# Optimization experiments

Hardware: AMD Instinct MI355X
Metric: run time of the kernel (lower is better)

Reference implementation:

```python
import jax, jax.numpy as jnp
import numpy as np

# dataset '25' constants
NBC = 30; DX = 10; NT = 1000; DT = 0.0008; FREQ = 25
SX = np.linspace(0, 99, num=10) * 10.0
SZ = 10.0
GX = np.linspace(0, 99, num=100) * 10.0
GZ = 10.0
SAMPLE_RATIO = 1
C1, C2, C3 = -2.5, 4.0 / 3.0, -1.0 / 12.0


def ricker(f, dt, nt):
    nw = 2.2 / f / dt
    nw = 2 * np.floor(nw / 2) + 1
    nc = np.floor(nw / 2)
    k = np.arange(nw)
    alpha = (nc - k) * f * dt * np.pi
    beta = alpha ** 2
    w0 = (1 - 2 * beta) * np.exp(-beta)
    w = np.zeros(nt)
    w[: len(w0)] = w0
    return jnp.asarray(w, dtype=jnp.float32)


def get_abc(vp, nbc, dx):
    B = vp.shape[0]
    velmin = jnp.min(vp.reshape(B, -1), axis=-1)              # [B]
    a = (nbc - 1) * dx
    kappa = 3.0 * velmin * np.float32(np.log(1e7)) / (2.0 * a)  # [B]
    prof = kappa[:, None] * (jnp.arange(nbc, dtype=vp.dtype) * dx / a) ** 2  # [B, nbc]
    pf = prof[:, ::-1]
    damp = jnp.zeros_like(vp)
    damp = damp.at[:, :, :nbc, :].set(pf[:, None, :, None])
    damp = damp.at[:, :, -nbc:, :].set(prof[:, None, :, None])
    damp = damp.at[:, :, :, :nbc].set(pf[:, None, None, :])
    damp = damp.at[:, :, :, -nbc:].set(prof[:, None, None, :])
    return damp


def fwm(v):
    # v: padded velocity [B, 1, nz_pad, nx_pad]
    src = ricker(FREQ, DT, NT)                                # [NT]
    alpha = (v * DT / DX) ** 2
    kappa = get_abc(v, NBC, DX) * DT
    temp1 = 2.0 + 2.0 * C1 * alpha - kappa
    temp2 = 1.0 - kappa
    beta_dt = (v * DT) ** 2

    isx = (np.around(SX / DX) + NBC).astype(int)              # [ns]
    isz = int(np.around(SZ / DX)) + NBC
    igx = (np.around(GX / DX) + NBC).astype(int)              # [ng]
    igz = int(np.around(GZ / DX)) + NBC
    ns = len(isx)

    B, nz, nx = v.shape[0], v.shape[2], v.shape[3]
    src_amp = beta_dt[:, 0, isz, isx]                         # [B, ns]
    loc = jnp.arange(ns)
    isx_j = jnp.asarray(isx)

    def step(carry, s):
        p0, p1 = carry                                        # each [B, ns, nz, nx]
        lap = C2 * (jnp.roll(p1, 1, -2) + jnp.roll(p1, -1, -2)
                    + jnp.roll(p1, 1, -1) + jnp.roll(p1, -1, -1)) \
            + C3 * (jnp.roll(p1, 2, -2) + jnp.roll(p1, -2, -2)
                    + jnp.roll(p1, 2, -1) + jnp.roll(p1, -2, -1))
        p = temp1 * p1 - temp2 * p0 + alpha * lap
        p = p.at[:, loc, isz, isx_j].add(src_amp * s)         # per-shot source injection
        rec = p[:, :, igz, igx]                               # [B, ns, ng]
        return (p1, p), rec

    p_init = jnp.zeros((B, ns, nz, nx), v.dtype)
    _, recs = jax.lax.scan(step, (p_init, p_init), src)       # recs: [NT, B, ns, ng]
    seis = jnp.transpose(recs, (1, 2, 0, 3))[:, :, ::SAMPLE_RATIO, :]
    return seis


def setup_inputs() -> dict:
    key = jax.random.key(0)
    v = jax.random.uniform(key, (1, 1, 70, 100), dtype=jnp.float32)
    return {"v": v}


def reference(v):
    v_denorm = v * 1000.0 + 3000.0                            # v_denorm_func
    v_pad = jnp.pad(v_denorm, ((0, 0), (0, 0), (NBC, NBC), (NBC, NBC)), mode="edge")
    seis = fwm(v_pad)                                         # [B, ns, NT, ng]
    return seis                                               # s_norm_func = identity
```

## Files before the change

kernel.cpp:

```cpp
#include <hip/hip_runtime.h>
#include <math.h>


#define SROW 168
#define PS_ROWS 52
#define PSZ (PS_ROWS * SROW)
#define RH 2
#define DTf 0.0008f
#define C2f 1.3333333333333333f
#define C3f (-0.08333333333333333f)

#define CST_OFF 4096
#define G_OFF   262144
#define FLAG_OFF 3590144
#define GSEG 10400

#define LD4(arr, i) (*reinterpret_cast<const float4*>(&(arr)[i]))
#define LD2(arr, i) (*reinterpret_cast<const float2*>(&(arr)[i]))
#define ST4(arr, i, v) (*reinterpret_cast<float4*>(&(arr)[i]) = (v))

__global__ __launch_bounds__(1024) void fwi_setup1(const float* __restrict__ v,
                                                   float* __restrict__ ws,
                                                   unsigned int* __restrict__ flags) {
    int tid = threadIdx.x;
    if (tid < 80) flags[tid] = 0u;
    float m = 3.402823466e38f;
    for (int i = tid; i < 7000; i += 1024) m = fminf(m, v[i]);
    #pragma unroll
    for (int off = 32; off > 0; off >>= 1) m = fminf(m, __shfl_down(m, off, 64));
    __shared__ float red[16];
    if ((tid & 63) == 0) red[tid >> 6] = m;
    __syncthreads();
    if (tid == 0) {
        float mm = red[0];
        for (int i = 1; i < 16; ++i) mm = fminf(mm, red[i]);
        ws[1010] = mm * 1000.0f + 3000.0f;
    }
    if (tid < 1000) {
        float w = 0.0f;
        if (tid < 111) {
            float a = (float)(55 - tid) * 0.06283185307179587f;
            float b = a * a;
            w = (1.0f - 2.0f * b) * expf(-b);
        }
        ws[tid] = w;
    }
    if (tid >= 1000 && tid < 1010) {
        int l = tid - 1000;
        float vd = v[100 + 11 * l] * 1000.0f + 3000.0f;
        float bdt = vd * DTf;
        ws[tid] = bdt * bdt;
    }
}

__global__ __launch_bounds__(256) void fwi_setup2(const float* __restrict__ v,
                                                  const float* __restrict__ ws,
                                                  float* __restrict__ CST) {
    int c = blockIdx.x * 256 + threadIdx.x;
    if (c >= 130 * 160) return;
    float velmin = ws[1010];
    int z = c / 160;
    int x = c - z * 160;
    int iz = min(max(z - 30, 0), 69);
    int ix = min(max(x - 30, 0), 99);
    float vd = v[iz * 100 + ix] * 1000.0f + 3000.0f;
    float tt = vd * DTf / 10.0f;
    float al = tt * tt;
    int qx = max(29 - x, x - 130);
    int qz = max(29 - z, z - 100);
    int q = (qx >= 0) ? qx : qz;
    float kdt = 0.0f;
    if (q >= 0) {
        float kap3 = 3.0f * velmin * 16.118095650958319f / 580.0f;
        float r = (float)q * (10.0f / 290.0f);
        kdt = kap3 * (r * r) * DTf;
    }
    int quad = c >> 2, j = c & 3;
    CST[quad * 12 + j]     = al;
    CST[quad * 12 + 4 + j] = 2.0f - 5.0f * al - kdt;
    CST[quad * 12 + 8 + j] = kdt - 1.0f;
}

static __device__ __forceinline__ float cellq(float l2, float l1, float cc, float r1, float r2,
                                              float u1, float u2, float d1, float d2,
                                              float al, float t1, float t2n, float p0) {
    float lap = C2f * ((l1 + r1) + (u1 + d1)) + C3f * ((l2 + r2) + (u2 + d2));
    return (t1 * cc + t2n * p0) + al * lap;
}

static __device__ __forceinline__ float4 ld_remote16(const unsigned long long* p) {
    union { unsigned long long u; float2 f; } a, b;
    a.u = __hip_atomic_load(p,     __ATOMIC_RELAXED, __HIP_MEMORY_SCOPE_AGENT);
    b.u = __hip_atomic_load(p + 1, __ATOMIC_RELAXED, __HIP_MEMORY_SCOPE_AGENT);
    return make_float4(a.f.x, a.f.y, b.f.x, b.f.y);
}
static __device__ __forceinline__ void st_remote16(unsigned long long* p, float4 v) {
    union { unsigned long long u; float2 f; } c;
    c.f = make_float2(v.x, v.y);
    __hip_atomic_store(p,     c.u, __ATOMIC_RELAXED, __HIP_MEMORY_SCOPE_AGENT);
    c.f = make_float2(v.z, v.w);
    __hip_atomic_store(p + 1, c.u, __ATOMIC_RELAXED, __HIP_MEMORY_SCOPE_AGENT);
}

#define ROWQ4(q, c, p0, hl, hr, u1, u2, d1, d2, al4, t14, t24) do {             \
    (q).x = cellq((hl).x, (hl).y, (c).x, (c).y, (c).z,                          \
                  (u1).x, (u2).x, (d1).x, (d2).x, (al4).x, (t14).x, (t24).x, (p0).x); \
    (q).y = cellq((hl).y, (c).x, (c).y, (c).z, (c).w,                           \
                  (u1).y, (u2).y, (d1).y, (d2).y, (al4).y, (t14).y, (t24).y, (p0).y); \
    (q).z = cellq((c).x, (c).y, (c).z, (c).w, (hr).x,                           \
                  (u1).z, (u2).z, (d1).z, (d2).z, (al4).z, (t14).z, (t24).z, (p0).z); \
    (q).w = cellq((c).y, (c).z, (c).w, (hr).x, (hr).y,                          \
                  (u1).w, (u2).w, (d1).w, (d2).w, (al4).w, (t14).w, (t24).w, (p0).w); \
} while (0)

#define STEP(CUR, OLD, T, K, PR, PW) do {                                       \
    const int Ti = (T);                                                         \
    const int kp1 = (K) + 1;                                                    \
    const bool actk = act && (gr >= (ct ? kp1 : 0)) && (gr < ng - (cb ? kp1 : 0)); \
    const float as = (Ti < 111) ? amp * Wv[Ti] : 0.0f;                          \
    if (actk) {                                                                 \
        float4 hu2 = LD4(PR, pc0 - 2 * SROW);                                   \
        float4 hu1 = LD4(PR, pc0 - SROW);                                       \
        float4 hd1 = LD4(PR, pc0 + 2 * SROW);                                   \
        float4 hd2 = LD4(PR, pc0 + 3 * SROW);                                   \
        float2 hl0 = LD2(PR, pc0 - 2);                                          \
        float2 hr0 = LD2(PR, pc0 + 4);                                          \
        float2 hl1 = LD2(PR, pc0 + SROW - 2);                                   \
        float2 hr1 = LD2(PR, pc0 + SROW + 4);                                   \
        float4 q0, q1;                                                          \
        ROWQ4(q0, (CUR)[0], (OLD)[0], hl0, hr0, hu1, hu2, (CUR)[1], hd1, ca0, ct0, cs0); \
        ROWQ4(q1, (CUR)[1], (OLD)[1], hl1, hr1, (CUR)[0], hu1, hd1, hd2, ca1, ct1, cs1); \
        if (src0) {                                 \
            q0.x += (ls == 0) ? as : 0.0f;                                      \
            q0.y += (ls == 1) ? as : 0.0f;                                      \
            q0.z += (ls == 2) ? as : 0.0f;                                      \
            q0.w += (ls == 3) ? as : 0.0f;                                      \
        }                                                                       \
        if (src1) {                                 \
            q1.x += (ls == 0) ? as : 0.0f;                                      \
            q1.y += (ls == 1) ? as : 0.0f;                                      \
            q1.z += (ls == 2) ? as : 0.0f;                                      \
            q1.w += (ls == 3) ? as : 0.0f;                                      \
        }                                                                       \
        if (grec) {                                 \
            const int ob = shot * 100000 + Ti * 100 + xr0;                      \
            if (xr0 >= 0  && xr0 <= 99) out[ob]     = q1.x;                     \
            if (xr0 >= -1 && xr0 <= 98) out[ob + 1] = q1.y;                     \
            if (xr0 >= -2 && xr0 <= 97) out[ob + 2] = q1.z;                     \
            if (xr0 >= -3 && xr0 <= 96) out[ob + 3] = q1.w;                     \
        }                                                                       \
        (OLD)[0] = q0; (OLD)[1] = q1;                                           \
        ST4(PW, pc0, q0);                                                       \
        ST4(PW, pc0 + SROW, q1);                                                \
    }                                                                           \
    __syncthreads();                            \
} while (0)

#define EXCHANGE(E) do {                                                        \
    const int par = (E) & 1;                                                    \
    if (act) {                                                                  \
        _Pragma("unroll")                                                       \
        for (int r = 0; r < RH; ++r) {                                          \
            int slot = gr * 2 + r;                                              \
            if (slot >= halo_top && slot < halo_top + int_n) {                  \
                int grow = base + slot;                                         \
                size_t b1 = ((size_t)(par*2+0)*10 + shot)*GSEG + (size_t)grow*80 + 2*qx; \
                size_t b0 = ((size_t)(par*2+1)*10 + shot)*GSEG + (size_t)grow*80 + 2*qx; \
                st_remote16(Gu + b1, pB[r]);                                    \
                st_remote16(Gu + b0, pA[r]);                                    \
            }                                                                   \
        }                                                                       \
    }                                                                           \
    __syncthreads();                                       \
    if (tid == 0)                                                               \
        __hip_atomic_store(&flags[(shot << 3) + seg], (unsigned)(E) + 1u,       \
                           __ATOMIC_RELEASE, __HIP_MEMORY_SCOPE_AGENT);         \
    if (tid == 64 && seg > 0)                                                   \
        while (__hip_atomic_load(&flags[(shot << 3) + seg - 1], __ATOMIC_ACQUIRE,\
                                 __HIP_MEMORY_SCOPE_AGENT) <= (unsigned)(E)) {} \
    if (tid == 128 && seg < 7)                                                  \
        while (__hip_atomic_load(&flags[(shot << 3) + seg + 1], __ATOMIC_ACQUIRE,\
                                 __HIP_MEMORY_SCOPE_AGENT) <= (unsigned)(E)) {} \
    __syncthreads();                                 \
    if (act) {                                                                  \
        _Pragma("unroll")                                                       \
        for (int r = 0; r < RH; ++r) {                                          \
            int slot = gr * 2 + r;                                              \
            if (slot < halo_top || slot >= halo_top + int_n) {                  \
                int grow = base + slot;                                         \
                size_t b1 = ((size_t)(par*2+0)*10 + shot)*GSEG + (size_t)grow*80 + 2*qx; \
                size_t b0 = ((size_t)(par*2+1)*10 + shot)*GSEG + (size_t)grow*80 + 2*qx; \
                float4 v1 = ld_remote16(Gu + b1);                               \
                float4 v0 = ld_remote16(Gu + b0);                               \
                pB[r] = v1;                                                     \
                pA[r] = v0;                                                     \
                ST4(PsA, pc0 + r * SROW, v1);                                   \
            }                                                                   \
        }                                                                       \
    }                                                                           \
    __syncthreads();                             \
} while (0)

__global__ __launch_bounds__(1024, 4) void fwi_main(const float4* __restrict__ CST4,
                                                    const float* __restrict__ ws,
                                                    unsigned long long* __restrict__ Gu,
                                                    unsigned int* __restrict__ flags,
                                                    float* __restrict__ out) {
    __shared__ float PsA[PSZ];
    __shared__ float PsB[PSZ];
    __shared__ float Wv[1024];
    const int tid = threadIdx.x;
    const int bid = blockIdx.x;
    const int shot = bid >> 3, seg = bid & 7;

    for (int i = tid; i < PSZ; i += 1024) { PsA[i] = 0.0f; PsB[i] = 0.0f; }
    Wv[tid] = (tid < 111) ? ws[tid] : 0.0f;

    const int int_base = 16 * seg;
    const int int_n = (seg < 7) ? 16 : 18;
    const int base = (seg > 0) ? int_base - 16 : 0;
    const int halo_top = (seg > 0) ? 16 : 0;
    const int stored_n = halo_top + int_n + ((seg < 7) ? 16 : 0);
    const bool ct = (seg > 0);
    const bool cb = (seg < 7);
    const int ng = stored_n >> 1;

    const int gr = tid / 40;
    const int qx = tid - gr * 40;
    const bool act = (gr < 24) && (gr * 2 < stored_n);
    const float amp = ws[1000 + shot];
    const int xs = 30 + 11 * shot;
    const bool isq = (qx == (xs >> 2));
    const int ls = xs & 3;
    const int s31 = 31 - base;
    const bool src0 = act && isq && (gr * 2 == s31);
    const bool src1 = act && isq && (gr * 2 + 1 == s31);
    const int pc0 = (gr * 2 + 2) * SROW + 4 * qx + 4;
    const float4* cst = CST4 + (size_t)((base + gr * 2) * 40 + qx) * 3;
    const bool grec = (seg == 1) && (gr == 15);
    const int xr0 = 4 * qx - 30;

    float4 ca0, ct0, cs0, ca1, ct1, cs1;
    ca0 = ct0 = cs0 = ca1 = ct1 = cs1 = make_float4(0.f, 0.f, 0.f, 0.f);
    if (act) {
        ca0 = cst[0];   ct0 = cst[1];   cs0 = cst[2];
        ca1 = cst[120]; ct1 = cst[121]; cs1 = cst[122];
    }

    float4 pA[RH], pB[RH];
    #pragma unroll
    for (int r = 0; r < RH; ++r) {
        pA[r] = make_float4(0.f, 0.f, 0.f, 0.f);
        pB[r] = make_float4(0.f, 0.f, 0.f, 0.f);
    }
    __syncthreads();

    for (int e = 0; e < 125; ++e) {
        #pragma unroll
        for (int kk = 0; kk < 4; ++kk) {
            STEP(pB, pA, e * 8 + 2 * kk,     2 * kk,     PsA, PsB);
            STEP(pA, pB, e * 8 + 2 * kk + 1, 2 * kk + 1, PsB, PsA);
        }
        if (e < 124) EXCHANGE(e);
    }
}

extern "C" void kernel_launch(void* const* d_in, const int* in_sizes, int n_in,
                              void* d_out, int out_size, void* d_ws, size_t ws_size,
                              hipStream_t stream) {
    const float* v = (const float*)d_in[0];
    float* ws = (float*)d_ws;
    float* CST = (float*)((char*)d_ws + CST_OFF);
    unsigned long long* Gu = (unsigned long long*)((char*)d_ws + G_OFF);
    unsigned int* flags = (unsigned int*)((char*)d_ws + FLAG_OFF);
    float* out = (float*)d_out;

    fwi_setup1<<<1, 1024, 0, stream>>>(v, ws, flags);
    fwi_setup2<<<82, 256, 0, stream>>>(v, ws, CST);
    fwi_main<<<80, 1024, 0, stream>>>((const float4*)CST, ws, Gu, flags, out);
}
```

Baseline: 1.277 ms.

## Fuse halo export into last step and let halo threads poll neighbor flags directly

The halo rows are now written to the global exchange buffer inside the last time step of each 8-step block, straight from the freshly computed registers. This removes the separate export pass and one block-wide barrier from the exchange. Instead of two designated threads spinning on the neighbor flags and then a barrier, each halo thread now polls its own neighbor's flag and loads its halo rows itself. This cuts barriers per exchange, but many threads now spin on atomics at once, and the release ordering now relies on the step barrier that comes before the flag store.

```diff
diff --git a/kernel.cpp b/kernel.cpp
--- a/kernel.cpp
+++ b/kernel.cpp
@@ -113,7 +113,7 @@
                   (u1).w, (u2).w, (d1).w, (d2).w, (al4).w, (t14).w, (t24).w, (p0).w); \
 } while (0)
 
-#define STEP(CUR, OLD, T, K, PR, PW) do {                                       \
+#define STEP(CUR, OLD, T, K, EXPF, EPAR, PR, PW) do {                           \
     const int Ti = (T);                                                         \
     const int kp1 = (K) + 1;                                                    \
     const bool actk = act && (gr >= (ct ? kp1 : 0)) && (gr < ng - (cb ? kp1 : 0)); \
@@ -149,54 +149,38 @@
             if (xr0 >= -2 && xr0 <= 97) out[ob + 2] = q1.z;                     \
             if (xr0 >= -3 && xr0 <= 96) out[ob + 3] = q1.w;                     \
         }                                                                       \
+        if ((EXPF) && exp01) {                         \
+            const size_t po = (size_t)((EPAR) * 20) * GSEG;                     \
+            st_remote16(Gu + po + eb0, q0);                                     \
+            st_remote16(Gu + po + (size_t)10 * GSEG + eb0, (CUR)[0]);           \
+            st_remote16(Gu + po + eb1, q1);                                     \
+            st_remote16(Gu + po + (size_t)10 * GSEG + eb1, (CUR)[1]);           \
+        }                                                                       \
         (OLD)[0] = q0; (OLD)[1] = q1;                                           \
         ST4(PW, pc0, q0);                                                       \
         ST4(PW, pc0 + SROW, q1);                                                \
     }                                                                           \
-    __syncthreads();                            \
+    __syncthreads();             \
 } while (0)
 
 #define EXCHANGE(E) do {                                                        \
     const int par = (E) & 1;                                                    \
-    if (act) {                                                                  \
-        _Pragma("unroll")                                                       \
-        for (int r = 0; r < RH; ++r) {                                          \
-            int slot = gr * 2 + r;                                              \
-            if (slot >= halo_top && slot < halo_top + int_n) {                  \
-                int grow = base + slot;                                         \
-                size_t b1 = ((size_t)(par*2+0)*10 + shot)*GSEG + (size_t)grow*80 + 2*qx; \
-                size_t b0 = ((size_t)(par*2+1)*10 + shot)*GSEG + (size_t)grow*80 + 2*qx; \
-                st_remote16(Gu + b1, pB[r]);                                    \
-                st_remote16(Gu + b0, pA[r]);                                    \
-            }                                                                   \
-        }                                                                       \
-    }                                                                           \
-    __syncthreads();                                       \
+    const size_t po1 = (size_t)(par * 20) * GSEG;                               \
+    const size_t po0 = po1 + (size_t)10 * GSEG;                                 \
     if (tid == 0)                                                               \
         __hip_atomic_store(&flags[(shot << 3) + seg], (unsigned)(E) + 1u,       \
                            __ATOMIC_RELEASE, __HIP_MEMORY_SCOPE_AGENT);         \
-    if (tid == 64 && seg > 0)                                                   \
-        while (__hip_atomic_load(&flags[(shot << 3) + seg - 1], __ATOMIC_ACQUIRE,\
+    if (act && halo_thr) {                                                      \
+        while (__hip_atomic_load(&flags[nbf], __ATOMIC_ACQUIRE,                 \
                                  __HIP_MEMORY_SCOPE_AGENT) <= (unsigned)(E)) {} \
-    if (tid == 128 && seg < 7)                                                  \
-        while (__hip_atomic_load(&flags[(shot << 3) + seg + 1], __ATOMIC_ACQUIRE,\
-                                 __HIP_MEMORY_SCOPE_AGENT) <= (unsigned)(E)) {} \
-    __syncthreads();                                 \
-    if (act) {                                                                  \
-        _Pragma("unroll")                                                       \
-        for (int r = 0; r < RH; ++r) {                                          \
-            int slot = gr * 2 + r;                                              \
-            if (slot < halo_top || slot >= halo_top + int_n) {                  \
-                int grow = base + slot;                                         \
-                size_t b1 = ((size_t)(par*2+0)*10 + shot)*GSEG + (size_t)grow*80 + 2*qx; \
-                size_t b0 = ((size_t)(par*2+1)*10 + shot)*GSEG + (size_t)grow*80 + 2*qx; \
-                float4 v1 = ld_remote16(Gu + b1);                               \
-                float4 v0 = ld_remote16(Gu + b0);                               \
-                pB[r] = v1;                                                     \
-                pA[r] = v0;                                                     \
-                ST4(PsA, pc0 + r * SROW, v1);                                   \
-            }                                                                   \
-        }                                                                       \
+        float4 v1a = ld_remote16(Gu + po1 + eb0);                               \
+        float4 v0a = ld_remote16(Gu + po0 + eb0);                               \
+        float4 v1b = ld_remote16(Gu + po1 + eb1);                               \
+        float4 v0b = ld_remote16(Gu + po0 + eb1);                               \
+        pB[0] = v1a; pA[0] = v0a;                                               \
+        pB[1] = v1b; pA[1] = v0b;                                               \
+        ST4(PsA, pc0, v1a);                                                     \
+        ST4(PsA, pc0 + SROW, v1b);                                              \
     }                                                                           \
     __syncthreads();                             \
 } while (0)
@@ -240,6 +224,15 @@
     const bool grec = (seg == 1) && (gr == 15);
     const int xr0 = 4 * qx - 30;
 
+    const int slot0 = gr * 2;
+    const bool exp01 = (slot0 >= halo_top) && (slot0 < halo_top + int_n);
+    const bool top_h = (slot0 < halo_top);
+    const bool bot_h = (slot0 >= halo_top + int_n) && (slot0 < stored_n);
+    const bool halo_thr = top_h || bot_h;
+    const int nbf = (shot << 3) + (top_h ? seg - 1 : seg + 1);
+    const size_t eb0 = (size_t)shot * GSEG + (size_t)(base + slot0) * 80 + 2 * qx;
+    const size_t eb1 = eb0 + 80;
+
     float4 ca0, ct0, cs0, ca1, ct1, cs1;
     ca0 = ct0 = cs0 = ca1 = ct1 = cs1 = make_float4(0.f, 0.f, 0.f, 0.f);
     if (act) {
@@ -258,8 +251,8 @@
     for (int e = 0; e < 125; ++e) {
         #pragma unroll
         for (int kk = 0; kk < 4; ++kk) {
-            STEP(pB, pA, e * 8 + 2 * kk,     2 * kk,     PsA, PsB);
-            STEP(pA, pB, e * 8 + 2 * kk + 1, 2 * kk + 1, PsB, PsA);
+            STEP(pB, pA, e * 8 + 2 * kk,     2 * kk,     false,      0,     PsA, PsB);
+            STEP(pA, pB, e * 8 + 2 * kk + 1, 2 * kk + 1, (kk == 3), (e & 1), PsB, PsA);
         }
         if (e < 124) EXCHANGE(e);
     }
```

Result: slower. 1.670 ms (+30.8%).
